# Performance work log

Measured on AMD Instinct MI355X. Metric: run time of the kernel, lower is better.

## Reference

```python
import jax, jax.numpy as jnp
import numpy as np

B = 1024
IN_SHAPE = ((8, 8, 8), (8, 8))
IN_RANKS = ((32, 32, 32), (32, 32))
OUT_SHAPE = (16, 16, 16)
OUT_RANK = (32, 32, 32)


def _xavier(key, shape):
    # xavier_normal over axes [0,1] (in) and [2] (out), matching the torch helper
    fan_in = shape[0] * shape[1]
    fan_out = shape[2]
    std = float(np.sqrt(2.0 / (fan_in + fan_out)))
    return jax.random.normal(key, shape, dtype=jnp.float32) * std


def setup_inputs() -> dict:
    key = jax.random.key(0)
    ks = jax.random.split(key, 12)
    x_dims = tuple(d for g in IN_SHAPE for d in g)
    inp = {"x": jax.random.normal(ks[0], (B,) + x_dims, dtype=jnp.float32)}
    # input TT factors, flattened over groups in order (group, mode)
    fac_shapes = []
    for shapes, ranks in zip(IN_SHAPE, IN_RANKS):
        for i in range(len(shapes)):
            r_prev = 1 if i == 0 else ranks[i - 1]
            fac_shapes.append((r_prev, shapes[i], ranks[i]))
    for idx, fs in enumerate(fac_shapes):
        inp[f"f{idx}"] = _xavier(ks[1 + idx], fs)
    # core: (last rank of each group..., output_rank[-1])
    core_shape = tuple(r[-1] for r in IN_RANKS) + (OUT_RANK[-1],)
    fan_in = int(np.prod(core_shape[:-1]))
    std = float(np.sqrt(2.0 / (fan_in + core_shape[-1])))
    inp["core"] = jax.random.normal(ks[6], core_shape, dtype=jnp.float32) * std
    # output TT factors
    for i in range(len(OUT_SHAPE)):
        r_prev = 1 if i == 0 else OUT_RANK[i - 1]
        inp[f"g{i}"] = _xavier(ks[7 + i], (r_prev, OUT_SHAPE[i], OUT_RANK[i]))
    # bias: uniform(-1/sqrt(fan_in), +) with fan_in = total input features
    total_in = int(np.prod([np.prod(s) for s in IN_SHAPE]))
    bound = 1.0 / float(np.sqrt(total_in))
    inp["bias"] = jax.random.uniform(ks[10], OUT_SHAPE, dtype=jnp.float32,
                                     minval=-bound, maxval=bound)
    return inp


def reference(x, f0, f1, f2, f3, f4, core, g0, g1, g2, bias):
    groups = ((f0, f1, f2), (f3, f4))
    Bsz = x.shape[0]
    # T: [B, remaining_modes_flat, accumulated_group_ranks_flat]
    T = x.reshape(Bsz, -1)[:, :, None]
    for facs in groups:
        first = facs[0][0]                       # squeeze dummy rank-1: [n, r]
        n = first.shape[0]
        T = T.reshape(Bsz, n, -1, T.shape[-1])   # [B, n, M', Racc]
        T = jnp.einsum("bnmq,nr->bmqr", T, first)  # [B, M', Racc, r]
        for f in facs[1:]:
            n = f.shape[1]
            T = T.reshape(Bsz, n, -1, T.shape[-2], T.shape[-1])
            T = jnp.einsum("bnmqp,pnr->bmqr", T, f)
        # fold this group's final rank into the accumulated rank axis
        T = T.reshape(Bsz, T.shape[1], -1)
    # all input modes consumed -> T is [B, 1, r1_last*r2_last]
    z = T.reshape(Bsz, -1) @ core.reshape(-1, core.shape[-1])  # [B, Rout]
    # output TT chain -> W[o0, o1, o2, R_last]
    W = g0[0]
    for g in (g1, g2):
        W = jnp.einsum("...p,poq->...oq", W, g)
    R = W.shape[-1]
    out = z @ W.reshape(-1, R).T                 # [B, prod(OUT_SHAPE)]
    out = out.reshape((Bsz,) + OUT_SHAPE)
    return out + bias
```

## Files before the change

kernel.cpp:

```cpp
#include <hip/hip_runtime.h>

#define WS_M2 0
#define WS_N2 16384
#define WS_WT 18432
#define WS_Z  149504

__global__ __launch_bounds__(256) void precompute_kernel(
    const float* __restrict__ f0, const float* __restrict__ f1,
    const float* __restrict__ f2, const float* __restrict__ f3,
    const float* __restrict__ f4, const float* __restrict__ g0,
    const float* __restrict__ g1, const float* __restrict__ g2,
    float* __restrict__ ws)
{
    __shared__ float sA[8192];
    const int t = threadIdx.x;
    const int blk = blockIdx.x;
    if (blk < 8) {
        for (int i = t; i < 2048; i += 256) {
            int a01 = i >> 5, r2 = i & 31;
            int a0 = a01 >> 3, a1 = a01 & 7;
            float s = 0.f;
            #pragma unroll
            for (int r1 = 0; r1 < 32; ++r1)
                s += f0[a0*32 + r1] * f1[r1*256 + a1*32 + r2];
            sA[i] = s;
        }
        __syncthreads();
        for (int i = t; i < 2048; i += 256) {
            int a012 = blk*64 + (i >> 5), r3 = i & 31;
            int a01 = a012 >> 3, a2 = a012 & 7;
            float s = 0.f;
            #pragma unroll
            for (int r2 = 0; r2 < 32; ++r2)
                s += sA[a01*32 + r2] * f2[r2*256 + a2*32 + r3];
            ws[WS_M2 + a012*32 + r3] = s;
        }
    } else if (blk == 8) {
        for (int i = t; i < 2048; i += 256) {
            int a34 = i >> 5, s2 = i & 31;
            int a3 = a34 >> 3, a4 = a34 & 7;
            float s = 0.f;
            #pragma unroll
            for (int s1 = 0; s1 < 32; ++s1)
                s += f3[a3*32 + s1] * f4[s1*256 + a4*32 + s2];
            ws[WS_N2 + i] = s;
        }
    } else {
        const int j = blk - 9;
        for (int i = t; i < 8192; i += 256) {
            int o01 = i >> 5, q = i & 31;
            int o0 = o01 >> 4, o1 = o01 & 15;
            float s = 0.f;
            #pragma unroll
            for (int p = 0; p < 32; ++p)
                s += g0[o0*32 + p] * g1[p*512 + o1*32 + q];
            sA[i] = s;
        }
        __syncthreads();
        for (int i = t; i < 4096; i += 256) {
            int o = j*128 + (i >> 5);
            int r = i & 31;
            int o01 = o >> 4, o2 = o & 15;
            float s = 0.f;
            #pragma unroll
            for (int q = 0; q < 32; ++q)
                s += sA[o01*32 + q] * g2[q*512 + o2*32 + r];
            ws[WS_WT + r*4096 + o] = s;
        }
    }
}

__global__ __launch_bounds__(256, 4) void main_kernel(
    const float* __restrict__ x, const float* __restrict__ core,
    const float* __restrict__ ws, float* __restrict__ zout)
{
    __shared__ float buf[8192];
    __shared__ float spart[512];
    const int t = threadIdx.x;
    const int b = blockIdx.x;

    const int tk = t >> 6;
    const int tm = (t >> 3) & 7;
    const int tr = t & 7;

    float4* buf4 = (float4*)buf;
    const float4* x4  = (const float4*)(x + (size_t)b * 32768);
    const float4* m24 = (const float4*)(ws + WS_M2);

    float acc[8][4];
    #pragma unroll
    for (int i = 0; i < 8; ++i)
        #pragma unroll
        for (int j = 0; j < 4; ++j) acc[i][j] = 0.f;

    for (int c = 0; c < 8; ++c) {
        const float4* xs = x4 + c*1024;
        #pragma unroll
        for (int i = 0; i < 4; ++i) buf4[i*256 + t] = xs[i*256 + t];
        const float4* ms = m24 + c*512;
        #pragma unroll
        for (int i = 0; i < 2; ++i) buf4[1024 + i*256 + t] = ms[i*256 + t];
        __syncthreads();

        #pragma unroll 4
        for (int k0 = 0; k0 < 16; ++k0) {
            const int k = tk*16 + k0;
            float4 xa = buf4[k*16 + tm*2];
            float4 xb = buf4[k*16 + tm*2 + 1];
            float4 wv = buf4[1024 + k*8 + tr];
            const float xm[8] = {xa.x,xa.y,xa.z,xa.w, xb.x,xb.y,xb.z,xb.w};
            #pragma unroll
            for (int i = 0; i < 8; ++i) {
                acc[i][0] += xm[i]*wv.x; acc[i][1] += xm[i]*wv.y;
                acc[i][2] += xm[i]*wv.z; acc[i][3] += xm[i]*wv.w;
            }
        }
        __syncthreads();
    }

    #pragma unroll
    for (int i = 0; i < 8; ++i) {
        float4 v = {acc[i][0], acc[i][1], acc[i][2], acc[i][3]};
        buf4[tk*512 + (tm*8 + i)*8 + tr] = v;
    }
    __syncthreads();

    {
        float4 s0 = buf4[t*2], s1 = buf4[t*2 + 1];
        #pragma unroll
        for (int q = 1; q < 4; ++q) {
            float4 a = buf4[q*512 + t*2], c2 = buf4[q*512 + t*2 + 1];
            s0.x+=a.x; s0.y+=a.y; s0.z+=a.z; s0.w+=a.w;
            s1.x+=c2.x; s1.y+=c2.y; s1.z+=c2.z; s1.w+=c2.w;
        }
        __syncthreads();
        buf4[t*2] = s0; buf4[t*2 + 1] = s1;
        const float4* n24 = (const float4*)(ws + WS_N2);
        buf4[512 + t] = n24[t];
        buf4[768 + t] = n24[256 + t];
    }
    __syncthreads();

    {
        const int r3  = t >> 3;
        const int s2b = (t & 7) * 4;
        float a0=0.f, a1=0.f, a2=0.f, a3=0.f;
        #pragma unroll 8
        for (int m = 0; m < 64; ++m) {
            float av = buf[m*32 + r3];
            const float* n = &buf[2048 + m*32 + s2b];
            a0 += av*n[0]; a1 += av*n[1]; a2 += av*n[2]; a3 += av*n[3];
        }
        float* d = &buf[4096 + r3*32 + s2b];
        d[0]=a0; d[1]=a1; d[2]=a2; d[3]=a3;
    }
    __syncthreads();

    {
        const int ro2 = t & 15;
        const int kc  = t >> 4;
        const float2* core2 = (const float2*)core;
        float s0 = 0.f, s1 = 0.f;
        const int k0 = kc * 64;
        for (int k = k0; k < k0 + 64; ++k) {
            float tv = buf[4096 + k];
            float2 cv = core2[k*16 + ro2];
            s0 += tv*cv.x; s1 += tv*cv.y;
        }
        spart[kc*32 + ro2*2 + 0] = s0;
        spart[kc*32 + ro2*2 + 1] = s1;
    }
    __syncthreads();
    if (t < 32) {
        float s = 0.f;
        #pragma unroll
        for (int kc = 0; kc < 16; ++kc) s += spart[kc*32 + t];
        zout[b*32 + t] = s;
    }
}

__global__ __launch_bounds__(256) void out_kernel(
    const float* __restrict__ ws, const float* __restrict__ bias,
    float* __restrict__ out)
{
    __shared__ float sW[8192];
    __shared__ float sZt[2176];
    __shared__ float sB[256];
    const int t  = threadIdx.x;
    const int bt = blockIdx.x;
    const int ot = blockIdx.y;

    {
        const float4* wt4 = (const float4*)(ws + WS_WT);
        float4* d = (float4*)sW;
        #pragma unroll
        for (int i = 0; i < 8; ++i) {
            int idx = i*256 + t;
            int ro = idx >> 6, oc = idx & 63;
            d[idx] = wt4[ro*1024 + ot*64 + oc];
        }
    }
    {
        const float4* z4 = (const float4*)(ws + WS_Z) + bt*512;
        #pragma unroll
        for (int i = 0; i < 2; ++i) {
            int idx = i*256 + t;
            int bl = idx >> 3, r4 = idx & 7;
            float4 v = z4[idx];
            sZt[(r4*4 + 0)*68 + bl] = v.x;
            sZt[(r4*4 + 1)*68 + bl] = v.y;
            sZt[(r4*4 + 2)*68 + bl] = v.z;
            sZt[(r4*4 + 3)*68 + bl] = v.w;
        }
    }
    if (t < 64) {
        const float4* b4 = (const float4*)bias + ot*64;
        ((float4*)sB)[t] = b4[t];
    }
    __syncthreads();

    const int oc = t & 63;
    const int bg = t >> 6;
    const float4* sW4 = (const float4*)sW;
    const float4 bv = ((const float4*)sB)[oc];
    float4* out4 = (float4*)out;

    for (int bi = 0; bi < 16; bi += 4) {
        const int bl = bg*16 + bi;
        float4 a0 = bv, a1 = bv, a2 = bv, a3 = bv;
        #pragma unroll
        for (int ro = 0; ro < 32; ++ro) {
            float4 w = sW4[ro*64 + oc];
            float4 z = *(const float4*)&sZt[ro*68 + bl];
            a0.x += z.x*w.x; a0.y += z.x*w.y; a0.z += z.x*w.z; a0.w += z.x*w.w;
            a1.x += z.y*w.x; a1.y += z.y*w.y; a1.z += z.y*w.z; a1.w += z.y*w.w;
            a2.x += z.z*w.x; a2.y += z.z*w.y; a2.z += z.z*w.z; a2.w += z.z*w.w;
            a3.x += z.w*w.x; a3.y += z.w*w.y; a3.z += z.w*w.z; a3.w += z.w*w.w;
        }
        const size_t obase = (size_t)(bt*64 + bl) * 1024 + ot*64 + oc;
        out4[obase + 0*1024] = a0;
        out4[obase + 1*1024] = a1;
        out4[obase + 2*1024] = a2;
        out4[obase + 3*1024] = a3;
    }
}

extern "C" void kernel_launch(void* const* d_in, const int* in_sizes, int n_in,
                              void* d_out, int out_size, void* d_ws, size_t ws_size,
                              hipStream_t stream)
{
    const float* x    = (const float*)d_in[0];
    const float* f0   = (const float*)d_in[1];
    const float* f1   = (const float*)d_in[2];
    const float* f2   = (const float*)d_in[3];
    const float* f3   = (const float*)d_in[4];
    const float* f4   = (const float*)d_in[5];
    const float* core = (const float*)d_in[6];
    const float* g0   = (const float*)d_in[7];
    const float* g1   = (const float*)d_in[8];
    const float* g2   = (const float*)d_in[9];
    const float* bias = (const float*)d_in[10];
    float* ws  = (float*)d_ws;
    float* out = (float*)d_out;

    precompute_kernel<<<41, 256, 0, stream>>>(f0, f1, f2, f3, f4, g0, g1, g2, ws);
    main_kernel<<<1024, 256, 0, stream>>>(x, core, ws, ws + WS_Z);
    out_kernel<<<dim3(16, 16), 256, 0, stream>>>(ws, bias, out);
}
```

Before: 266.4 us.

## Stream x directly from global with wave-uniform M2 loads instead of LDS staging

The first contraction stage no longer stages x and M2 tiles through shared memory with per-chunk barriers. Each wave now owns a quarter of the K dimension, each lane loads its x column straight from global memory, and the M2 rows are read with wave-uniform addresses so they can become scalar loads. Every lane keeps 32 accumulators for the rank dimension. Partial sums are written to a padded (stride 65) LDS layout and reduced across waves. This removes the LDS traffic and barriers of the main loop, at the cost of more registers per thread and uncoalesced-looking strided x loads (stride 64 floats across iterations, coalesced across lanes).

New measurement: 264.3 us. Within noise of the previous version (-0.8%).

```diff
diff --git a/kernel.cpp b/kernel.cpp
--- a/kernel.cpp
+++ b/kernel.cpp
@@ -74,70 +74,55 @@
     const float* __restrict__ x, const float* __restrict__ core,
     const float* __restrict__ ws, float* __restrict__ zout)
 {
-    __shared__ float buf[8192];
+    __shared__ float buf[8320];
     __shared__ float spart[512];
     const int t = threadIdx.x;
     const int b = blockIdx.x;
-
-    const int tk = t >> 6;
-    const int tm = (t >> 3) & 7;
-    const int tr = t & 7;
-
-    float4* buf4 = (float4*)buf;
-    const float4* x4  = (const float4*)(x + (size_t)b * 32768);
-    const float4* m24 = (const float4*)(ws + WS_M2);
-
-    float acc[8][4];
+    const int w    = __builtin_amdgcn_readfirstlane(t >> 6);
+    const int lane = t & 63;
+
+    const float* __restrict__ xw = x + (size_t)b * 32768 + w * 8192 + lane;
+    const float* __restrict__ m2 = ws + WS_M2 + w * 4096;
+
+    float acc[32];
     #pragma unroll
-    for (int i = 0; i < 8; ++i)
-        #pragma unroll
-        for (int j = 0; j < 4; ++j) acc[i][j] = 0.f;
-
-    for (int c = 0; c < 8; ++c) {
-        const float4* xs = x4 + c*1024;
-        #pragma unroll
-        for (int i = 0; i < 4; ++i) buf4[i*256 + t] = xs[i*256 + t];
-        const float4* ms = m24 + c*512;
-        #pragma unroll
-        for (int i = 0; i < 2; ++i) buf4[1024 + i*256 + t] = ms[i*256 + t];
-        __syncthreads();
-
-        #pragma unroll 4
-        for (int k0 = 0; k0 < 16; ++k0) {
-            const int k = tk*16 + k0;
-            float4 xa = buf4[k*16 + tm*2];
-            float4 xb = buf4[k*16 + tm*2 + 1];
-            float4 wv = buf4[1024 + k*8 + tr];
-            const float xm[8] = {xa.x,xa.y,xa.z,xa.w, xb.x,xb.y,xb.z,xb.w};
-            #pragma unroll
-            for (int i = 0; i < 8; ++i) {
-                acc[i][0] += xm[i]*wv.x; acc[i][1] += xm[i]*wv.y;
-                acc[i][2] += xm[i]*wv.z; acc[i][3] += xm[i]*wv.w;
-            }
-        }
-        __syncthreads();
+    for (int r = 0; r < 32; ++r) acc[r] = 0.f;
+
+    for (int k0 = 0; k0 < 128; k0 += 8) {
+        float xv[8];
+        #pragma unroll
+        for (int i = 0; i < 8; ++i) xv[i] = xw[(k0 + i) * 64];
+        #pragma unroll
+        for (int i = 0; i < 8; ++i) {
+            const float* __restrict__ mr = m2 + (k0 + i) * 32;
+            #pragma unroll
+            for (int r = 0; r < 32; ++r) acc[r] += xv[i] * mr[r];
+        }
     }
 
     #pragma unroll
-    for (int i = 0; i < 8; ++i) {
-        float4 v = {acc[i][0], acc[i][1], acc[i][2], acc[i][3]};
-        buf4[tk*512 + (tm*8 + i)*8 + tr] = v;
-    }
-    __syncthreads();
-
-    {
-        float4 s0 = buf4[t*2], s1 = buf4[t*2 + 1];
-        #pragma unroll
-        for (int q = 1; q < 4; ++q) {
-            float4 a = buf4[q*512 + t*2], c2 = buf4[q*512 + t*2 + 1];
-            s0.x+=a.x; s0.y+=a.y; s0.z+=a.z; s0.w+=a.w;
-            s1.x+=c2.x; s1.y+=c2.y; s1.z+=c2.z; s1.w+=c2.w;
-        }
-        __syncthreads();
-        buf4[t*2] = s0; buf4[t*2 + 1] = s1;
+    for (int r = 0; r < 32; ++r) buf[w*2080 + r*65 + lane] = acc[r];
+    __syncthreads();
+
+    {
+        const int rr = t >> 3;
+        const int mb = (t & 7) * 8;
+        float s[8];
+        #pragma unroll
+        for (int i = 0; i < 8; ++i) {
+            s[i] = buf[rr*65 + mb + i] + buf[2080 + rr*65 + mb + i]
+                 + buf[4160 + rr*65 + mb + i] + buf[6240 + rr*65 + mb + i];
+        }
+        #pragma unroll
+        for (int i = 0; i < 8; ++i) buf[rr*65 + mb + i] = s[i];
+    }
+    __syncthreads();
+
+    {
         const float4* n24 = (const float4*)(ws + WS_N2);
-        buf4[512 + t] = n24[t];
-        buf4[768 + t] = n24[256 + t];
+        float4* d = (float4*)(buf + 4160);
+        d[t] = n24[t];
+        d[256 + t] = n24[256 + t];
     }
     __syncthreads();
 
@@ -147,11 +132,11 @@
         float a0=0.f, a1=0.f, a2=0.f, a3=0.f;
         #pragma unroll 8
         for (int m = 0; m < 64; ++m) {
-            float av = buf[m*32 + r3];
-            const float* n = &buf[2048 + m*32 + s2b];
+            float av = buf[r3*65 + m];
+            const float* n = &buf[4160 + m*32 + s2b];
             a0 += av*n[0]; a1 += av*n[1]; a2 += av*n[2]; a3 += av*n[3];
         }
-        float* d = &buf[4096 + r3*32 + s2b];
+        float* d = &buf[6240 + r3*32 + s2b];
         d[0]=a0; d[1]=a1; d[2]=a2; d[3]=a3;
     }
     __syncthreads();
@@ -163,7 +148,7 @@
         float s0 = 0.f, s1 = 0.f;
         const int k0 = kc * 64;
         for (int k = k0; k < k0 + 64; ++k) {
-            float tv = buf[4096 + k];
+            float tv = buf[6240 + k];
             float2 cv = core2[k*16 + ro2];
             s0 += tv*cv.x; s1 += tv*cv.y;
         }
```
